# Kernel tuning notes

Hardware: AMD Instinct MI355X
Metric: run time of the kernel (lower is better)

## Reference

```python
import jax, jax.numpy as jnp
import numpy as np

B, N, FIN, F = 512, 512, 2, 128  # batch, n_sites, input features, hidden features


def setup_inputs() -> dict:
    key = jax.random.key(0)
    k1, k2 = jax.random.split(key)
    inputs = jax.random.normal(k1, (B, N, FIN), dtype=jnp.float32)
    # LSTM dense kernel over concat([inputs_i, hidden]) -> 4*F gates (i, f, g, o)
    Wk = jax.random.normal(k2, (FIN + F, 4 * F), dtype=jnp.float32) / np.sqrt(FIN + F)
    b = jnp.zeros((4 * F,), dtype=jnp.float32)
    return {"inputs": inputs, "Wk": Wk, "b": b}


def reference(inputs, Wk, b):
    # exclusive=True, reorder_idx=None: inputs_i = 0 at k=0, else inputs[:, k-1, :];
    # memory state = outputs[:, k-1, :] = previous hidden (zeros buffer at k=0).
    batch = inputs.shape[0]
    x_shift = jnp.concatenate(
        [jnp.zeros_like(inputs[:, :1, :]), inputs[:, :-1, :]], axis=1
    )  # (B, N, FIN)
    xs = jnp.swapaxes(x_shift, 0, 1)  # (N, B, FIN) scan over sites

    c0 = jnp.zeros((batch, F), dtype=inputs.dtype)
    h0 = jnp.zeros((batch, F), dtype=inputs.dtype)

    def step(carry, x_t):
        c, h = carry
        ifgo = jnp.concatenate([x_t, h], axis=-1) @ Wk + b  # (B, 4F)
        i, f, g, o = jnp.split(ifgo, 4, axis=-1)
        c = jax.nn.sigmoid(f) * c + jax.nn.sigmoid(i) * jnp.tanh(g)
        h = jax.nn.sigmoid(o) * jnp.tanh(c)
        return (c, h), h

    _, hs = jax.lax.scan(step, (c0, h0), xs)  # hs: (N, B, F)
    outputs = jnp.swapaxes(hs, 0, 1)  # (B, N, F)
    return outputs
```

## Files before the change

kernel.cpp:

```cpp
#include <hip/hip_runtime.h>

#define B_   512
#define N_   512
#define FIN_ 2
#define F_   128
#define G_   512
#define XSTRIDE 1040
#define HSTRIDE 160

typedef _Float16 half8  __attribute__((ext_vector_type(8)));
typedef float    float4_ __attribute__((ext_vector_type(4)));
typedef float    float2_ __attribute__((ext_vector_type(2)));

#define LOG2E_  1.44269504f
#define LOG2E2_ 2.88539008f

template<bool PF>
__device__ __forceinline__ void lstm_step(
    const _Float16* hsrc,
    _Float16* hdst,
    float* outp,
    const half8 (&wf)[4][4], const float (&w0r)[4], const float (&w1r)[4],
    const float (&br)[4], float4_ (&acc)[4], float2_ xv,
    float& cs, int grp, int rotofs,
    const float* xpf, float2_& pf1, float2_& pf2)
{
    half8 af[4];
#pragma unroll
    for (int i = 0; i < 4; ++i)
        af[i] = *reinterpret_cast<const half8*>(hsrc + ((i * 32) ^ rotofs) + grp * 8);

    if (PF) {
        pf1 = *reinterpret_cast<const float2_*>(xpf);
        pf2 = *reinterpret_cast<const float2_*>(xpf + 2);
    }

#pragma unroll
    for (int t = 0; t < 4; ++t)
        acc[t][0] = fmaf(xv[0], w0r[t], fmaf(xv[1], w1r[t], br[t]));

#pragma unroll
    for (int i = 0; i < 3; ++i)
#pragma unroll
        for (int t = 0; t < 4; ++t)
            acc[t] = __builtin_amdgcn_mfma_f32_16x16x32_f16(af[i], wf[t][i], acc[t], 0, 0, 0);
    acc[2] = __builtin_amdgcn_mfma_f32_16x16x32_f16(af[3], wf[2][3], acc[2], 0, 0, 0);
    acc[0] = __builtin_amdgcn_mfma_f32_16x16x32_f16(af[3], wf[0][3], acc[0], 0, 0, 0);
    acc[1] = __builtin_amdgcn_mfma_f32_16x16x32_f16(af[3], wf[1][3], acc[1], 0, 0, 0);
    acc[3] = __builtin_amdgcn_mfma_f32_16x16x32_f16(af[3], wf[3][3], acc[3], 0, 0, 0);

    const float eg = __builtin_amdgcn_exp2f(LOG2E2_ * acc[2][0]);
    const float ei = __builtin_amdgcn_exp2f(-LOG2E_ * acc[0][0]);
    const float ef = __builtin_amdgcn_exp2f(-LOG2E_ * acc[1][0]);
    const float rg = __builtin_amdgcn_rcpf(1.f + eg);
    const float ri = __builtin_amdgcn_rcpf(1.f + ei);
    const float rf = __builtin_amdgcn_rcpf(1.f + ef);
    const float gg = fmaf(-2.f, rg, 1.f);
    cs = fmaf(rf, cs, ri * gg);
    const float eo = __builtin_amdgcn_exp2f(-LOG2E_ * acc[3][0]);
    const float ec = __builtin_amdgcn_exp2f(LOG2E2_ * cs);
    const float ro = __builtin_amdgcn_rcpf(1.f + eo);
    const float rc = __builtin_amdgcn_rcpf(1.f + ec);
    const float h = fmaf(-2.f * ro, rc, ro);
    *hdst = (_Float16)h;
    *outp = h;
    asm volatile("s_waitcnt lgkmcnt(0)\n\ts_barrier" ::: "memory");
}

__global__ void __launch_bounds__(512)
lstm_scan(const float* __restrict__ inp, const float* __restrict__ Wk,
          const float* __restrict__ bias, float* __restrict__ out)
{
    const int bb   = blockIdx.x;
    const int tid  = threadIdx.x;
    const int w    = tid >> 6;
    const int lane = tid & 63;
    const int c15  = lane & 15;
    const int grp  = lane >> 4;
    const int rotofs = ((((w >> 2) ^ w) & 1) != 0) ? 64 : 0;

    __shared__ __align__(64) _Float16 h_lds[2][2 * HSTRIDE];
    __shared__ __align__(64) float    x_lds[2 * XSTRIDE];

    half8 wf[4][4];
    float w0r[4], w1r[4], br[4];
#pragma unroll
    for (int t = 0; t < 4; ++t) {
        const int col = t * F_ + w * 16 + c15;
        w0r[t] = Wk[col];
        w1r[t] = Wk[G_ + col];
        br[t]  = bias[col];
#pragma unroll
        for (int i = 0; i < 4; ++i) {
            half8 f;
#pragma unroll
            for (int e = 0; e < 8; ++e)
                f[e] = (_Float16)Wk[(size_t)(2 + ((i * 32) ^ rotofs) + grp * 8 + e) * G_ + col];
            wf[t][i] = f;
        }
    }

    {
        const float* xsrc = inp + (size_t)(2 * bb) * (N_ * FIN_);
        const int i4 = tid * 4;
        float4_ v = *reinterpret_cast<const float4_*>(xsrc + i4);
        const int row = i4 >> 10, idx = i4 & 1023;
        *reinterpret_cast<float4_*>(&x_lds[row * XSTRIDE + idx]) = v;
    }
    for (int i = tid; i < 2 * 2 * HSTRIDE; i += 512)
        ((_Float16*)h_lds)[i] = (_Float16)0.f;
    __syncthreads();

    const int r    = (lane >> 4) & 1;
    const int hrow = (c15 >> 2) & 1;

    const _Float16* hr0 = &h_lds[0][hrow * HSTRIDE];
    const _Float16* hr1 = &h_lds[1][hrow * HSTRIDE];
    _Float16* hw0 = &h_lds[0][r * HSTRIDE + w * 16 + c15];
    _Float16* hw1 = &h_lds[1][r * HSTRIDE + w * 16 + c15];
    const float* xq = &x_lds[r * XSTRIDE];
    float* outp = out + (size_t)(2 * bb + r) * N_ * F_ + w * 16 + c15;

    float cs = 0.f;
    float4_ acc[4];
#pragma unroll
    for (int t = 0; t < 4; ++t) { acc[t][0] = 0.f; acc[t][1] = 0.f; acc[t][2] = 0.f; acc[t][3] = 0.f; }

    float2_ xz; xz[0] = 0.f; xz[1] = 0.f;
    float2_ pf1, pf2;

    lstm_step<true>(hr0, hw1, outp, wf, w0r, w1r, br, acc, xz, cs, grp, rotofs,
                    xq, pf1, pf2);
    outp += F_;

    for (int i = 0; i < 255; ++i) {
        const float2_ xv1 = pf1;
        const float2_ xv2 = pf2;
        lstm_step<true>(hr1, hw0, outp, wf, w0r, w1r, br, acc, xv1, cs, grp,
                        rotofs, xq + 4 * i + 4, pf1, pf2);
        outp += F_;
        lstm_step<false>(hr0, hw1, outp, wf, w0r, w1r, br, acc, xv2, cs, grp,
                         rotofs, nullptr, pf1, pf2);
        outp += F_;
    }
    lstm_step<false>(hr1, hw0, outp, wf, w0r, w1r, br, acc, pf1, cs, grp,
                     rotofs, nullptr, pf1, pf2);
}

extern "C" void kernel_launch(void* const* d_in, const int* in_sizes, int n_in,
                              void* d_out, int out_size, void* d_ws, size_t ws_size,
                              hipStream_t stream) {
    const float* inp  = (const float*)d_in[0];
    const float* Wk   = (const float*)d_in[1];
    const float* bias = (const float*)d_in[2];
    float* out        = (float*)d_out;
    lstm_scan<<<dim3(B_ / 2), dim3(512), 0, stream>>>(inp, Wk, bias, out);
}
```

Measured before the change: 234.6 us.

## Quantize LSTM recurrent weights and hidden state to int8 MFMA

Replaces the fp16 16x16x32 MFMA recurrent matmul with int8 16x16x64 MFMA, quantizing the weights per column at kernel start and the hidden state at a fixed scale of 127 each step. This halves the MFMA count and LDS read width per step on the serial critical path. The input projection and bias are now added in fp32 after the integer accumulation, and the LDS hidden-state layout changes. It adds a per-thread weight max scan at startup and brings in int8 quantization error that builds up over 512 recurrent steps, which may break accuracy tolerance.

```diff
diff --git a/kernel.cpp b/kernel.cpp
--- a/kernel.cpp
+++ b/kernel.cpp
@@ -6,63 +6,69 @@
 #define F_   128
 #define G_   512
 #define XSTRIDE 1040
-#define HSTRIDE 160
+#define H8STRIDE 320
 
-typedef _Float16 half8  __attribute__((ext_vector_type(8)));
-typedef float    float4_ __attribute__((ext_vector_type(4)));
-typedef float    float2_ __attribute__((ext_vector_type(2)));
+typedef int         int4_   __attribute__((ext_vector_type(4)));
+typedef float       float4_ __attribute__((ext_vector_type(4)));
+typedef float       float2_ __attribute__((ext_vector_type(2)));
 
 #define LOG2E_  1.44269504f
 #define LOG2E2_ 2.88539008f
 
 template<bool PF>
 __device__ __forceinline__ void lstm_step(
-    const _Float16* hsrc,
-    _Float16* hdst,
+    const signed char* hsrc,
+    signed char* hdst,
     float* outp,
-    const half8 (&wf)[4][4], const float (&w0r)[4], const float (&w1r)[4],
-    const float (&br)[4], float4_ (&acc)[4], float2_ xv,
-    float& cs, int grp, int rotofs,
+    const int4_ (&wq)[4][2], const float (&invs)[4],
+    const float (&w0r)[4], const float (&w1r)[4], const float (&br)[4],
+    int4_ (&acc)[4], float2_ xv, float& cs, int grp,
     const float* xpf, float2_& pf1, float2_& pf2)
 {
-    half8 af[4];
-#pragma unroll
-    for (int i = 0; i < 4; ++i)
-        af[i] = *reinterpret_cast<const half8*>(hsrc + ((i * 32) ^ rotofs) + grp * 8);
+    const int4_ a0 = *reinterpret_cast<const int4_*>(hsrc + grp * 16);
+    const int4_ a1 = *reinterpret_cast<const int4_*>(hsrc + 64 + grp * 16);
 
     if (PF) {
         pf1 = *reinterpret_cast<const float2_*>(xpf);
         pf2 = *reinterpret_cast<const float2_*>(xpf + 2);
     }
 
+    float xp[4];
 #pragma unroll
     for (int t = 0; t < 4; ++t)
-        acc[t][0] = fmaf(xv[0], w0r[t], fmaf(xv[1], w1r[t], br[t]));
+        xp[t] = fmaf(xv[0], w0r[t], fmaf(xv[1], w1r[t], br[t]));
 
 #pragma unroll
-    for (int i = 0; i < 3; ++i)
+    for (int t = 0; t < 4; ++t) acc[t][0] = 0;
+
 #pragma unroll
-        for (int t = 0; t < 4; ++t)
-            acc[t] = __builtin_amdgcn_mfma_f32_16x16x32_f16(af[i], wf[t][i], acc[t], 0, 0, 0);
-    acc[2] = __builtin_amdgcn_mfma_f32_16x16x32_f16(af[3], wf[2][3], acc[2], 0, 0, 0);
-    acc[0] = __builtin_amdgcn_mfma_f32_16x16x32_f16(af[3], wf[0][3], acc[0], 0, 0, 0);
-    acc[1] = __builtin_amdgcn_mfma_f32_16x16x32_f16(af[3], wf[1][3], acc[1], 0, 0, 0);
-    acc[3] = __builtin_amdgcn_mfma_f32_16x16x32_f16(af[3], wf[3][3], acc[3], 0, 0, 0);
+    for (int t = 0; t < 4; ++t)
+        acc[t] = __builtin_amdgcn_mfma_i32_16x16x64_i8(a0, wq[t][0], acc[t], 0, 0, 0);
+    acc[2] = __builtin_amdgcn_mfma_i32_16x16x64_i8(a1, wq[2][1], acc[2], 0, 0, 0);
+    acc[0] = __builtin_amdgcn_mfma_i32_16x16x64_i8(a1, wq[0][1], acc[0], 0, 0, 0);
+    acc[1] = __builtin_amdgcn_mfma_i32_16x16x64_i8(a1, wq[1][1], acc[1], 0, 0, 0);
+    acc[3] = __builtin_amdgcn_mfma_i32_16x16x64_i8(a1, wq[3][1], acc[3], 0, 0, 0);
 
-    const float eg = __builtin_amdgcn_exp2f(LOG2E2_ * acc[2][0]);
-    const float ei = __builtin_amdgcn_exp2f(-LOG2E_ * acc[0][0]);
-    const float ef = __builtin_amdgcn_exp2f(-LOG2E_ * acc[1][0]);
+    const float pg = fmaf((float)acc[2][0], invs[2], xp[2]);
+    const float pi = fmaf((float)acc[0][0], invs[0], xp[0]);
+    const float pf_ = fmaf((float)acc[1][0], invs[1], xp[1]);
+    const float eg = __builtin_amdgcn_exp2f(LOG2E2_ * pg);
+    const float ei = __builtin_amdgcn_exp2f(-LOG2E_ * pi);
+    const float ef = __builtin_amdgcn_exp2f(-LOG2E_ * pf_);
     const float rg = __builtin_amdgcn_rcpf(1.f + eg);
     const float ri = __builtin_amdgcn_rcpf(1.f + ei);
     const float rf = __builtin_amdgcn_rcpf(1.f + ef);
     const float gg = fmaf(-2.f, rg, 1.f);
     cs = fmaf(rf, cs, ri * gg);
-    const float eo = __builtin_amdgcn_exp2f(-LOG2E_ * acc[3][0]);
+    const float po = fmaf((float)acc[3][0], invs[3], xp[3]);
+    const float eo = __builtin_amdgcn_exp2f(-LOG2E_ * po);
     const float ec = __builtin_amdgcn_exp2f(LOG2E2_ * cs);
     const float ro = __builtin_amdgcn_rcpf(1.f + eo);
     const float rc = __builtin_amdgcn_rcpf(1.f + ec);
     const float h = fmaf(-2.f * ro, rc, ro);
-    *hdst = (_Float16)h;
+
+    const int q = (int)rintf(h * 127.f);
+    *hdst = (signed char)q;
     *outp = h;
     asm volatile("s_waitcnt lgkmcnt(0)\n\ts_barrier" ::: "memory");
 }
@@ -77,28 +83,41 @@
     const int lane = tid & 63;
     const int c15  = lane & 15;
     const int grp  = lane >> 4;
-    const int rotofs = ((((w >> 2) ^ w) & 1) != 0) ? 64 : 0;
 
-    __shared__ __align__(64) _Float16 h_lds[2][2 * HSTRIDE];
-    __shared__ __align__(64) float    x_lds[2 * XSTRIDE];
+    __shared__ __align__(16) signed char h8[2][4 * H8STRIDE];
+    __shared__ __align__(64) float x_lds[2 * XSTRIDE];
 
-    half8 wf[4][4];
-    float w0r[4], w1r[4], br[4];
+    float w0r[4], w1r[4], br[4], invs[4], scl[4];
+    int cols[4];
 #pragma unroll
     for (int t = 0; t < 4; ++t) {
         const int col = t * F_ + w * 16 + c15;
+        cols[t] = col;
         w0r[t] = Wk[col];
         w1r[t] = Wk[G_ + col];
         br[t]  = bias[col];
+        float cm = 1e-20f;
+        for (int k = 0; k < F_; ++k)
+            cm = fmaxf(cm, fabsf(Wk[(size_t)(2 + k) * G_ + col]));
+        scl[t]  = 127.f / cm;
+        invs[t] = cm / (127.f * 127.f);
+    }
+    int4_ wq[4][2];
 #pragma unroll
-        for (int i = 0; i < 4; ++i) {
-            half8 f;
+    for (int t = 0; t < 4; ++t)
 #pragma unroll
-            for (int e = 0; e < 8; ++e)
-                f[e] = (_Float16)Wk[(size_t)(2 + ((i * 32) ^ rotofs) + grp * 8 + e) * G_ + col];
-            wf[t][i] = f;
+        for (int i = 0; i < 2; ++i) {
+            union { int4_ v; signed char c[16]; } u;
+#pragma unroll
+            for (int e = 0; e < 16; ++e) {
+                const int k = i * 64 + grp * 16 + e;
+                const float wv = Wk[(size_t)(2 + k) * G_ + cols[t]] * scl[t];
+                int q = (int)rintf(wv);
+                q = q > 127 ? 127 : (q < -127 ? -127 : q);
+                u.c[e] = (signed char)q;
+            }
+            wq[t][i] = u.v;
         }
-    }
 
     {
         const float* xsrc = inp + (size_t)(2 * bb) * (N_ * FIN_);
@@ -107,44 +126,45 @@
         const int row = i4 >> 10, idx = i4 & 1023;
         *reinterpret_cast<float4_*>(&x_lds[row * XSTRIDE + idx]) = v;
     }
-    for (int i = tid; i < 2 * 2 * HSTRIDE; i += 512)
-        ((_Float16*)h_lds)[i] = (_Float16)0.f;
+    for (int i = tid; i < 2 * 4 * H8STRIDE; i += 512)
+        ((signed char*)h8)[i] = 0;
     __syncthreads();
 
     const int r    = (lane >> 4) & 1;
     const int hrow = (c15 >> 2) & 1;
+    const int wrow = r + ((lane >> 5) << 1);
 
-    const _Float16* hr0 = &h_lds[0][hrow * HSTRIDE];
-    const _Float16* hr1 = &h_lds[1][hrow * HSTRIDE];
-    _Float16* hw0 = &h_lds[0][r * HSTRIDE + w * 16 + c15];
-    _Float16* hw1 = &h_lds[1][r * HSTRIDE + w * 16 + c15];
+    const signed char* hr0 = &h8[0][hrow * H8STRIDE];
+    const signed char* hr1 = &h8[1][hrow * H8STRIDE];
+    signed char* hw0 = &h8[0][wrow * H8STRIDE + w * 16 + c15];
+    signed char* hw1 = &h8[1][wrow * H8STRIDE + w * 16 + c15];
     const float* xq = &x_lds[r * XSTRIDE];
     float* outp = out + (size_t)(2 * bb + r) * N_ * F_ + w * 16 + c15;
 
     float cs = 0.f;
-    float4_ acc[4];
+    int4_ acc[4];
 #pragma unroll
-    for (int t = 0; t < 4; ++t) { acc[t][0] = 0.f; acc[t][1] = 0.f; acc[t][2] = 0.f; acc[t][3] = 0.f; }
+    for (int t = 0; t < 4; ++t) { acc[t][0] = 0; acc[t][1] = 0; acc[t][2] = 0; acc[t][3] = 0; }
 
     float2_ xz; xz[0] = 0.f; xz[1] = 0.f;
     float2_ pf1, pf2;
 
-    lstm_step<true>(hr0, hw1, outp, wf, w0r, w1r, br, acc, xz, cs, grp, rotofs,
+    lstm_step<true>(hr0, hw1, outp, wq, invs, w0r, w1r, br, acc, xz, cs, grp,
                     xq, pf1, pf2);
     outp += F_;
 
     for (int i = 0; i < 255; ++i) {
         const float2_ xv1 = pf1;
         const float2_ xv2 = pf2;
-        lstm_step<true>(hr1, hw0, outp, wf, w0r, w1r, br, acc, xv1, cs, grp,
-                        rotofs, xq + 4 * i + 4, pf1, pf2);
+        lstm_step<true>(hr1, hw0, outp, wq, invs, w0r, w1r, br, acc, xv1, cs,
+                        grp, xq + 4 * i + 4, pf1, pf2);
         outp += F_;
-        lstm_step<false>(hr0, hw1, outp, wf, w0r, w1r, br, acc, xv2, cs, grp,
-                         rotofs, nullptr, pf1, pf2);
+        lstm_step<false>(hr0, hw1, outp, wq, invs, w0r, w1r, br, acc, xv2, cs,
+                         grp, nullptr, pf1, pf2);
         outp += F_;
     }
-    lstm_step<false>(hr1, hw0, outp, wf, w0r, w1r, br, acc, pf1, cs, grp,
-                     rotofs, nullptr, pf1, pf2);
+    lstm_step<false>(hr1, hw0, outp, wq, invs, w0r, w1r, br, acc, pf1, cs,
+                     grp, nullptr, pf1, pf2);
 }
 
 extern "C" void kernel_launch(void* const* d_in, const int* in_sizes, int n_in,
```

New measurement: 276.0 us. 17.7% more time.
